# Optimization experiments

Hardware: AMD Instinct MI355X
Metric: run time of the kernel (lower is better)

The kernel has to match this reference:

```python
import jax, jax.numpy as jnp
import numpy as np

HEADS = 4
DIM_HEAD = 32
GROUPS = 32  # min(256//4, 32)
EPS = 1e-5


def setup_inputs() -> dict:
    key = jax.random.key(0)
    ks = jax.random.split(key, 6)
    B, C, H, W = 16, 256, 64, 64
    hidden = HEADS * DIM_HEAD  # 128
    return {
        "x": jax.random.normal(ks[0], (B, C, H, W), dtype=jnp.float32),
        "gn_w": jax.random.uniform(ks[1], (C,), dtype=jnp.float32),
        "gn_b": jax.random.normal(ks[2], (C,), dtype=jnp.float32) * 0.05,
        "qkv_w": jax.random.normal(ks[3], (3 * hidden, C), dtype=jnp.float32) * 0.05,
        "qkv_b": jax.random.normal(ks[4], (3 * hidden,), dtype=jnp.float32) * 0.05,
        "out_w": jax.random.normal(ks[5], (C, hidden), dtype=jnp.float32) * 0.05,
        "out_b": jnp.zeros((C,), dtype=jnp.float32),
    }


def _forward_single(x, gn_w, gn_b, qkv_w, qkv_b, out_w, out_b):
    # x: (c, h, w)
    c, h, w = x.shape
    # GroupNorm over (channels-in-group, h, w)
    xg = x.reshape(GROUPS, c // GROUPS, h, w)
    mean = xg.mean(axis=(1, 2, 3), keepdims=True)
    var = xg.var(axis=(1, 2, 3), keepdims=True)
    xn = ((xg - mean) * jax.lax.rsqrt(var + EPS)).reshape(c, h, w)
    xn = xn * gn_w[:, None, None] + gn_b[:, None, None]
    # 1x1 conv QKV projection
    qkv = jnp.einsum('oc,chw->ohw', qkv_w, xn) + qkv_b[:, None, None]
    qkv = qkv.reshape(3, HEADS, DIM_HEAD, h * w)
    q, k, v = qkv[0], qkv[1], qkv[2]
    k = jax.nn.softmax(k, axis=-1)  # softmax over spatial
    context = jnp.einsum('hdn,hen->hde', k, v)   # (heads, d, d)
    out = jnp.einsum('hde,hdn->hen', context, q)  # (heads, d, n)
    out = out.reshape(HEADS * DIM_HEAD, h, w)
    # 1x1 conv output projection
    return jnp.einsum('oc,chw->ohw', out_w, out) + out_b[:, None, None]


def reference(x, gn_w, gn_b, qkv_w, qkv_b, out_w, out_b):
    f = lambda xi: _forward_single(xi, gn_w, gn_b, qkv_w, qkv_b, out_w, out_b)
    return jax.vmap(f)(x)
```

## Files before the change

kernel.cpp:

```cpp
#include <hip/hip_runtime.h>
#include <stdint.h>

typedef unsigned short u16;
typedef __attribute__((ext_vector_type(8))) short bf16x8;
typedef __attribute__((ext_vector_type(4))) float f32x4;

#define B_   16
#define C_   256
#define HW_  4096
#define QR_  384
#define HID_ 128

__device__ __forceinline__ float b2f(u16 u) {
  union { uint32_t i; float f; } v; v.i = ((uint32_t)u) << 16; return v.f;
}
__device__ __forceinline__ u16 f2b(float f) {
  union { float f; uint32_t i; } v; v.f = f;
  uint32_t r = (v.i + 0x7FFFu + ((v.i >> 16) & 1u)) >> 16;
  return (u16)r;
}

__global__ __launch_bounds__(256) void gn_stats_conv_kernel(
    const float* __restrict__ x, const float* __restrict__ gnw,
    const float* __restrict__ gnb, float* __restrict__ scale,
    float* __restrict__ shiftv,
    const float* __restrict__ qkvw, u16* __restrict__ cqkvw)
{
  if (blockIdx.x >= 512) {
    int i = (blockIdx.x - 512) * 256 + threadIdx.x;
    float4 f = ((const float4*)qkvw)[i];
    ushort4 o;
    o.x = f2b(f.x); o.y = f2b(f.y); o.z = f2b(f.z); o.w = f2b(f.w);
    ((ushort4*)cqkvw)[i] = o;
    return;
  }
  int b = blockIdx.x >> 5, g = blockIdx.x & 31;
  const float* p = x + ((size_t)b * C_ + g * 8) * HW_;
  int t = threadIdx.x;
  float s = 0.f, sq = 0.f;
#pragma unroll
  for (int i = 0; i < 16; ++i) {
    float4 u0 = *(const float4*)(p + t * 8 + i * 2048);
    float4 u1 = *(const float4*)(p + t * 8 + i * 2048 + 4);
    s  += u0.x + u0.y + u0.z + u0.w + u1.x + u1.y + u1.z + u1.w;
    sq += u0.x*u0.x + u0.y*u0.y + u0.z*u0.z + u0.w*u0.w
        + u1.x*u1.x + u1.y*u1.y + u1.z*u1.z + u1.w*u1.w;
  }
#pragma unroll
  for (int off = 32; off > 0; off >>= 1) {
    s  += __shfl_down(s, off);
    sq += __shfl_down(sq, off);
  }
  __shared__ float ps[4], pq[4], mr[2];
  int lane = t & 63, w = t >> 6;
  if (lane == 0) { ps[w] = s; pq[w] = sq; }
  __syncthreads();
  if (t == 0) {
    float S = ps[0] + ps[1] + ps[2] + ps[3];
    float Q = pq[0] + pq[1] + pq[2] + pq[3];
    float mean = S * (1.f / 32768.f);
    float var  = Q * (1.f / 32768.f) - mean * mean;
    mr[0] = mean; mr[1] = rsqrtf(var + 1e-5f);
  }
  __syncthreads();
  if (t < 8) {
    int c = g * 8 + t;
    float sc = gnw[c] * mr[1];
    scale[b * C_ + c]  = sc;
    shiftv[b * C_ + c] = gnb[c] - mr[0] * sc;
  }
}

__global__ __launch_bounds__(256) void gn_transpose_kernel(
    const float* __restrict__ x, u16* __restrict__ dst,
    const float* __restrict__ scale, const float* __restrict__ shiftv)
{
  int nt = blockIdx.x, ct = blockIdx.y, b = blockIdx.z;
  const float* S = x + (size_t)b * C_ * HW_;
  u16* D = dst + (size_t)b * HW_ * C_;
  __shared__ __align__(16) u16 tile[64][136];
  int t = threadIdx.x;
  int n0 = nt * 128, c0 = ct * 64;
  int r = t >> 2, seg = (t & 3) * 32;
  float sc = scale[(size_t)b * C_ + c0 + r];
  float sh = shiftv[(size_t)b * C_ + c0 + r];
#pragma unroll
  for (int i = 0; i < 4; ++i) {
    const float* rp = S + (size_t)(c0 + r) * HW_ + n0 + seg + i * 8;
    float4 u0 = *(const float4*)(rp);
    float4 u1 = *(const float4*)(rp + 4);
    float f[8] = {u0.x, u0.y, u0.z, u0.w, u1.x, u1.y, u1.z, u1.w};
    uint4 o;
    uint32_t* op = (uint32_t*)&o;
#pragma unroll
    for (int j = 0; j < 4; ++j) {
      op[j] = (uint32_t)f2b(f[2 * j] * sc + sh)
            | ((uint32_t)f2b(f[2 * j + 1] * sc + sh) << 16);
    }
    *(uint4*)&tile[r][seg + i * 8] = o;
  }
  __syncthreads();
#pragma unroll
  for (int i = 0; i < 4; ++i) {
    int m = t * 4 + i;
    int n_l = m >> 3, cg = (m & 7) * 8;
    union { u16 v[8]; uint4 q; } pk;
#pragma unroll
    for (int e = 0; e < 8; ++e) pk.v[e] = tile[cg + e][n_l];
    *(uint4*)(D + (size_t)(n0 + n_l) * C_ + c0 + cg) = pk.q;
  }
}

__global__ __launch_bounds__(256) void qkv_gemm_kernel(
    const u16* __restrict__ A, const u16* __restrict__ Bt,
    const float* __restrict__ bias, u16* __restrict__ qkv,
    u16* __restrict__ q_t)
{
  const int K = C_;
  int nt = blockIdx.x, mt = blockIdx.y, b = blockIdx.z;
  const u16* Ab = A + (size_t)mt * 128 * K;
  const u16* Bb = Bt + (size_t)b * HW_ * C_ + (size_t)nt * 128 * K;
  __shared__ __align__(16) u16 smem[128 * 136];
  u16* lA = smem;
  u16* lB = smem + 8192;
  int t = threadIdx.x;
  int lane = t & 63, w = t >> 6;
  int quad = lane >> 4, l16 = lane & 15;
  int wm = (w >> 1) * 64, wn = (w & 1) * 64;
  f32x4 acc[4][4];
#pragma unroll
  for (int i = 0; i < 4; ++i)
#pragma unroll
    for (int j = 0; j < 4; ++j)
#pragma unroll
      for (int r = 0; r < 4; ++r) acc[i][j][r] = 0.f;

  for (int k0 = 0; k0 < K; k0 += 64) {
    __syncthreads();
#pragma unroll
    for (int q = 0; q < 4; ++q) {
      int ch = q * 256 + t;
      int row = ch >> 3, off = (ch & 7) * 8;
      __builtin_amdgcn_global_load_lds(
          (const __attribute__((address_space(1))) void*)(Ab + (size_t)row * K + k0 + off),
          (__attribute__((address_space(3))) void*)(lA + ch * 8), 16, 0, 0);
      __builtin_amdgcn_global_load_lds(
          (const __attribute__((address_space(1))) void*)(Bb + (size_t)row * K + k0 + off),
          (__attribute__((address_space(3))) void*)(lB + ch * 8), 16, 0, 0);
    }
    __syncthreads();
    const bf16x8* A8 = (const bf16x8*)lA;
    const bf16x8* B8 = (const bf16x8*)lB;
#pragma unroll
    for (int kk = 0; kk < 2; ++kk) {
      bf16x8 af[4], bfr[4];
#pragma unroll
      for (int i = 0; i < 4; ++i) af[i]  = A8[(wm + i * 16 + l16) * 8 + kk * 4 + quad];
#pragma unroll
      for (int j = 0; j < 4; ++j) bfr[j] = B8[(wn + j * 16 + l16) * 8 + kk * 4 + quad];
#pragma unroll
      for (int i = 0; i < 4; ++i)
#pragma unroll
        for (int j = 0; j < 4; ++j)
          acc[i][j] = __builtin_amdgcn_mfma_f32_16x16x32_bf16(af[i], bfr[j],
                                                              acc[i][j], 0, 0, 0);
    }
  }

  if (mt == 0) {
    __syncthreads();
#pragma unroll
    for (int i = 0; i < 4; ++i) {
      int o0 = wm + i * 16 + quad * 4;
      float b0 = bias[o0], b1 = bias[o0 + 1], b2 = bias[o0 + 2], b3 = bias[o0 + 3];
#pragma unroll
      for (int j = 0; j < 4; ++j) {
        int n_l = wn + j * 16 + l16;
        uint2 pk;
        pk.x = (uint32_t)f2b(acc[i][j][0] + b0) | ((uint32_t)f2b(acc[i][j][1] + b1) << 16);
        pk.y = (uint32_t)f2b(acc[i][j][2] + b2) | ((uint32_t)f2b(acc[i][j][3] + b3) << 16);
        *(uint2*)&smem[n_l * 136 + o0] = pk;
      }
    }
    __syncthreads();
    int n_l = t >> 1, half = t & 1;
    u16* dst = q_t + (size_t)b * HW_ * HID_ + (size_t)(nt * 128 + n_l) * HID_ + half * 64;
    const u16* srcp = smem + n_l * 136 + half * 64;
#pragma unroll
    for (int i = 0; i < 8; ++i)
      *(uint4*)(dst + i * 8) = *(const uint4*)(srcp + i * 8);
  } else {
#pragma unroll
    for (int i = 0; i < 4; ++i) {
#pragma unroll
      for (int rg = 0; rg < 4; ++rg) {
        int o = mt * 128 + wm + i * 16 + quad * 4 + rg;
        float bsv = bias[o];
        size_t rowbase = (size_t)b * QR_ * HW_ + (size_t)o * HW_;
#pragma unroll
        for (int j = 0; j < 4; ++j) {
          int n = nt * 128 + wn + j * 16 + l16;
          qkv[rowbase + n] = f2b(acc[i][j][rg] + bsv);
        }
      }
    }
  }
}

__global__ __launch_bounds__(1024) void ctxwf_kernel(
    const u16* __restrict__ qkv, const float* __restrict__ outw,
    u16* __restrict__ wf)
{
  int b = blockIdx.x >> 2, h = blockIdx.x & 3;
  const u16* kb = qkv + ((size_t)b * QR_ + 128 + h * 32) * HW_;
  const u16* vb = qkv + ((size_t)b * QR_ + 256 + h * 32) * HW_;
  int t = threadIdx.x;
  int w = t >> 6, lane = t & 63;
  int quad = lane >> 4, l16 = lane & 15;
  __shared__ float part[16][1024];
  __shared__ float cs[1024];
  __shared__ float2 sred[1024];
  __shared__ float sinv[32];
  f32x4 acc[2][2];
#pragma unroll
  for (int i = 0; i < 2; ++i)
#pragma unroll
    for (int j = 0; j < 2; ++j)
#pragma unroll
      for (int r = 0; r < 4; ++r) acc[i][j][r] = 0.f;
  float s0 = 0.f, s1 = 0.f;
  int kbase = w * 256;
  for (int it = 0; it < 8; ++it) {
    int n0 = kbase + it * 32 + quad * 8;
    bf16x8 k0 = *(const bf16x8*)(kb + (size_t)l16 * HW_ + n0);
    bf16x8 k1 = *(const bf16x8*)(kb + (size_t)(16 + l16) * HW_ + n0);
    bf16x8 v0 = *(const bf16x8*)(vb + (size_t)l16 * HW_ + n0);
    bf16x8 v1 = *(const bf16x8*)(vb + (size_t)(16 + l16) * HW_ + n0);
    bf16x8 a0, a1;
    const u16* k0p = (const u16*)&k0; u16* a0p = (u16*)&a0;
    const u16* k1p = (const u16*)&k1; u16* a1p = (u16*)&a1;
#pragma unroll
    for (int e = 0; e < 8; ++e) {
      float e0 = __expf(b2f(k0p[e]));
      float e1 = __expf(b2f(k1p[e]));
      s0 += e0; s1 += e1;
      a0p[e] = f2b(e0);
      a1p[e] = f2b(e1);
    }
    acc[0][0] = __builtin_amdgcn_mfma_f32_16x16x32_bf16(a0, v0, acc[0][0], 0, 0, 0);
    acc[0][1] = __builtin_amdgcn_mfma_f32_16x16x32_bf16(a0, v1, acc[0][1], 0, 0, 0);
    acc[1][0] = __builtin_amdgcn_mfma_f32_16x16x32_bf16(a1, v0, acc[1][0], 0, 0, 0);
    acc[1][1] = __builtin_amdgcn_mfma_f32_16x16x32_bf16(a1, v1, acc[1][1], 0, 0, 0);
  }
#pragma unroll
  for (int i = 0; i < 2; ++i)
#pragma unroll
    for (int j = 0; j < 2; ++j)
#pragma unroll
      for (int r = 0; r < 4; ++r) {
        int d = i * 16 + quad * 4 + r;
        int e = j * 16 + l16;
        part[w][d * 32 + e] = acc[i][j][r];
      }
  sred[t] = make_float2(s0, s1);
  __syncthreads();
  {
    float a = 0.f;
#pragma unroll
    for (int ww = 0; ww < 16; ++ww) a += part[ww][t];
    cs[t] = a;
  }
  if (t < 32) {
    int d = t, lsel = d & 15;
    float ssum = 0.f;
#pragma unroll
    for (int ww = 0; ww < 16; ++ww)
#pragma unroll
      for (int q = 0; q < 4; ++q) {
        float2 v2 = sred[ww * 64 + q * 16 + lsel];
        ssum += (d < 16) ? v2.x : v2.y;
      }
    sinv[d] = 1.f / ssum;
  }
  __syncthreads();

  int o = t & 255, dg = t >> 8;
  const float* wr = outw + (size_t)o * HID_ + h * 32;
  float wv[32];
#pragma unroll
  for (int e = 0; e < 32; ++e) wv[e] = wr[e];
  union { u16 v[8]; uint4 q; } pk;
#pragma unroll
  for (int dd = 0; dd < 8; ++dd) {
    int d = dg * 8 + dd;
    float a = 0.f;
#pragma unroll
    for (int e = 0; e < 32; ++e) a += wv[e] * cs[d * 32 + e];
    pk.v[dd] = f2b(a * sinv[d]);
  }
  *(uint4*)(wf + ((size_t)b * C_ + o) * HID_ + h * 32 + dg * 8) = pk.q;
}

__global__ __launch_bounds__(256) void out_gemm_kernel(
    const u16* __restrict__ A, const u16* __restrict__ Bt,
    const float* __restrict__ bias, float* __restrict__ Cout)
{
  const int K = HID_;
  int nt = blockIdx.x, mt = blockIdx.y, b = blockIdx.z;
  const u16* Ab = A + (size_t)b * C_ * HID_ + (size_t)mt * 128 * K;
  const u16* Bb = Bt + (size_t)b * HW_ * HID_ + (size_t)nt * 128 * K;
  __shared__ __align__(16) u16 lA[128 * 64];
  __shared__ __align__(16) u16 lB[128 * 64];
  int t = threadIdx.x;
  int lane = t & 63, w = t >> 6;
  int quad = lane >> 4, l16 = lane & 15;
  int wm = (w >> 1) * 64, wn = (w & 1) * 64;
  f32x4 acc[4][4];
#pragma unroll
  for (int i = 0; i < 4; ++i)
#pragma unroll
    for (int j = 0; j < 4; ++j)
#pragma unroll
      for (int r = 0; r < 4; ++r) acc[i][j][r] = 0.f;

  for (int k0 = 0; k0 < K; k0 += 64) {
    __syncthreads();
#pragma unroll
    for (int q = 0; q < 4; ++q) {
      int ch = q * 256 + t;
      int row = ch >> 3, off = (ch & 7) * 8;
      __builtin_amdgcn_global_load_lds(
          (const __attribute__((address_space(1))) void*)(Ab + (size_t)row * K + k0 + off),
          (__attribute__((address_space(3))) void*)(lA + ch * 8), 16, 0, 0);
      __builtin_amdgcn_global_load_lds(
          (const __attribute__((address_space(1))) void*)(Bb + (size_t)row * K + k0 + off),
          (__attribute__((address_space(3))) void*)(lB + ch * 8), 16, 0, 0);
    }
    __syncthreads();
    const bf16x8* A8 = (const bf16x8*)lA;
    const bf16x8* B8 = (const bf16x8*)lB;
#pragma unroll
    for (int kk = 0; kk < 2; ++kk) {
      bf16x8 af[4], bfr[4];
#pragma unroll
      for (int i = 0; i < 4; ++i) af[i]  = A8[(wm + i * 16 + l16) * 8 + kk * 4 + quad];
#pragma unroll
      for (int j = 0; j < 4; ++j) bfr[j] = B8[(wn + j * 16 + l16) * 8 + kk * 4 + quad];
#pragma unroll
      for (int i = 0; i < 4; ++i)
#pragma unroll
        for (int j = 0; j < 4; ++j)
          acc[i][j] = __builtin_amdgcn_mfma_f32_16x16x32_bf16(af[i], bfr[j],
                                                              acc[i][j], 0, 0, 0);
    }
  }
#pragma unroll
  for (int i = 0; i < 4; ++i) {
#pragma unroll
    for (int rg = 0; rg < 4; ++rg) {
      int o = mt * 128 + wm + i * 16 + quad * 4 + rg;
      float bsv = bias[o];
      size_t rowbase = (size_t)b * C_ * HW_ + (size_t)o * HW_;
#pragma unroll
      for (int j = 0; j < 4; ++j) {
        int n = nt * 128 + wn + j * 16 + l16;
        Cout[rowbase + n] = acc[i][j][rg] + bsv;
      }
    }
  }
}

extern "C" void kernel_launch(void* const* d_in, const int* in_sizes, int n_in,
                              void* d_out, int out_size, void* d_ws, size_t ws_size,
                              hipStream_t stream)
{
  const float* x    = (const float*)d_in[0];
  const float* gnw  = (const float*)d_in[1];
  const float* gnb  = (const float*)d_in[2];
  const float* qkvw = (const float*)d_in[3];
  const float* qkvb = (const float*)d_in[4];
  const float* outw = (const float*)d_in[5];
  const float* outb = (const float*)d_in[6];

  char* p = (char*)d_ws;
  float* scale  = (float*)p;            p += (size_t)B_ * C_ * 4;
  float* shiftv = (float*)p;            p += (size_t)B_ * C_ * 4;
  u16* cqkvw = (u16*)p;                 p += (size_t)QR_ * C_ * 2;
  u16* xn_t  = (u16*)p;                 p += (size_t)B_ * HW_ * C_ * 2;
  u16* qkv   = (u16*)p;                 p += (size_t)B_ * QR_ * HW_ * 2;
  u16* q_t   = (u16*)p;                 p += (size_t)B_ * HW_ * HID_ * 2;
  u16* wf    = (u16*)p;

  gn_stats_conv_kernel<<<608, 256, 0, stream>>>(x, gnw, gnb, scale, shiftv,
                                                qkvw, cqkvw);
  gn_transpose_kernel<<<dim3(32, 4, 16), 256, 0, stream>>>(x, xn_t, scale, shiftv);
  qkv_gemm_kernel<<<dim3(32, 3, 16), 256, 0, stream>>>(cqkvw, xn_t, qkvb, qkv, q_t);
  ctxwf_kernel<<<64, 1024, 0, stream>>>(qkv, outw, wf);
  out_gemm_kernel<<<dim3(32, 2, 16), 256, 0, stream>>>(wf, q_t, outb, (float*)d_out);
}
```

Measured before the change: 206.9 us.

## Fuse K/V projection with softmax-exp and context accumulation, avoiding K/V materialisation

Splits the QKV GEMM into a Q-only GEMM and a new K/V kernel that computes K and V tiles, applies exp to K, and multiplies the tiles in shared memory to produce per-tile partial contexts and softmax sums. This removes the bf16 write and re-read of the full K/V tensors and spreads the context reduction over 512 blocks instead of 64. A small fold kernel then sums the partials, folds the V bias into the output-weight product and builds the fused weight. The cost is extra partial-buffer traffic and a third launch. K is computed without its bias, which is safe because softmax over spatial positions is unchanged by a per-row constant shift, so no max-subtraction is done.

```diff
diff --git a/kernel.cpp b/kernel.cpp
--- a/kernel.cpp
+++ b/kernel.cpp
@@ -111,14 +111,13 @@
   }
 }
 
-__global__ __launch_bounds__(256) void qkv_gemm_kernel(
+__global__ __launch_bounds__(256) void q_gemm_kernel(
     const u16* __restrict__ A, const u16* __restrict__ Bt,
-    const float* __restrict__ bias, u16* __restrict__ qkv,
-    u16* __restrict__ q_t)
+    const float* __restrict__ bias, u16* __restrict__ q_t)
 {
   const int K = C_;
-  int nt = blockIdx.x, mt = blockIdx.y, b = blockIdx.z;
-  const u16* Ab = A + (size_t)mt * 128 * K;
+  int nt = blockIdx.x, b = blockIdx.y;
+  const u16* Ab = A;
   const u16* Bb = Bt + (size_t)b * HW_ * C_ + (size_t)nt * 128 * K;
   __shared__ __align__(16) u16 smem[128 * 136];
   u16* lA = smem;
@@ -167,138 +166,228 @@
     }
   }
 
-  if (mt == 0) {
-    __syncthreads();
-#pragma unroll
-    for (int i = 0; i < 4; ++i) {
-      int o0 = wm + i * 16 + quad * 4;
-      float b0 = bias[o0], b1 = bias[o0 + 1], b2 = bias[o0 + 2], b3 = bias[o0 + 3];
-#pragma unroll
-      for (int j = 0; j < 4; ++j) {
-        int n_l = wn + j * 16 + l16;
-        uint2 pk;
-        pk.x = (uint32_t)f2b(acc[i][j][0] + b0) | ((uint32_t)f2b(acc[i][j][1] + b1) << 16);
-        pk.y = (uint32_t)f2b(acc[i][j][2] + b2) | ((uint32_t)f2b(acc[i][j][3] + b3) << 16);
-        *(uint2*)&smem[n_l * 136 + o0] = pk;
+  __syncthreads();
+#pragma unroll
+  for (int i = 0; i < 4; ++i) {
+    int o0 = wm + i * 16 + quad * 4;
+    float b0 = bias[o0], b1 = bias[o0 + 1], b2 = bias[o0 + 2], b3 = bias[o0 + 3];
+#pragma unroll
+    for (int j = 0; j < 4; ++j) {
+      int n_l = wn + j * 16 + l16;
+      uint2 pk;
+      pk.x = (uint32_t)f2b(acc[i][j][0] + b0) | ((uint32_t)f2b(acc[i][j][1] + b1) << 16);
+      pk.y = (uint32_t)f2b(acc[i][j][2] + b2) | ((uint32_t)f2b(acc[i][j][3] + b3) << 16);
+      *(uint2*)&smem[n_l * 136 + o0] = pk;
+    }
+  }
+  __syncthreads();
+  int n_l = t >> 1, half = t & 1;
+  u16* dst = q_t + (size_t)b * HW_ * HID_ + (size_t)(nt * 128 + n_l) * HID_ + half * 64;
+  const u16* srcp = smem + n_l * 136 + half * 64;
+#pragma unroll
+  for (int i = 0; i < 8; ++i)
+    *(uint4*)(dst + i * 8) = *(const uint4*)(srcp + i * 8);
+}
+
+__global__ __launch_bounds__(512) void kv_ctx_kernel(
+    const u16* __restrict__ A,
+    const u16* __restrict__ Bt,
+    float* __restrict__ ctx_part,
+    float* __restrict__ s_part)
+{
+  const int K = C_;
+  int nt = blockIdx.x, b = blockIdx.y;
+  const u16* Ab = A;
+  const u16* Bb = Bt + (size_t)b * HW_ * C_ + (size_t)nt * 128 * K;
+  __shared__ __align__(16) union {
+    struct { u16 lA[256 * 64]; u16 lB[128 * 64]; } st;
+    struct { u16 ek[128][136]; u16 vv[128][136]; float sred[2][128]; } ep;
+    float cred[4096];
+  } sm;
+  int t = threadIdx.x;
+  int lane = t & 63, w = t >> 6;
+  int quad = lane >> 4, l16 = lane & 15;
+  int wm = (w >> 1) * 64, wn = (w & 1) * 64;
+  f32x4 acc[4][4];
+#pragma unroll
+  for (int i = 0; i < 4; ++i)
+#pragma unroll
+    for (int j = 0; j < 4; ++j)
+#pragma unroll
+      for (int r = 0; r < 4; ++r) acc[i][j][r] = 0.f;
+
+  for (int k0 = 0; k0 < K; k0 += 64) {
+    __syncthreads();
+#pragma unroll
+    for (int q = 0; q < 4; ++q) {
+      int ch = q * 512 + t;
+      int row = ch >> 3, off = (ch & 7) * 8;
+      __builtin_amdgcn_global_load_lds(
+          (const __attribute__((address_space(1))) void*)(Ab + (size_t)row * K + k0 + off),
+          (__attribute__((address_space(3))) void*)(sm.st.lA + ch * 8), 16, 0, 0);
+    }
+#pragma unroll
+    for (int q = 0; q < 2; ++q) {
+      int ch = q * 512 + t;
+      int row = ch >> 3, off = (ch & 7) * 8;
+      __builtin_amdgcn_global_load_lds(
+          (const __attribute__((address_space(1))) void*)(Bb + (size_t)row * K + k0 + off),
+          (__attribute__((address_space(3))) void*)(sm.st.lB + ch * 8), 16, 0, 0);
+    }
+    __syncthreads();
+    const bf16x8* A8 = (const bf16x8*)sm.st.lA;
+    const bf16x8* B8 = (const bf16x8*)sm.st.lB;
+#pragma unroll
+    for (int kk = 0; kk < 2; ++kk) {
+      bf16x8 af[4], bfr[4];
+#pragma unroll
+      for (int i = 0; i < 4; ++i) af[i]  = A8[(wm + i * 16 + l16) * 8 + kk * 4 + quad];
+#pragma unroll
+      for (int j = 0; j < 4; ++j) bfr[j] = B8[(wn + j * 16 + l16) * 8 + kk * 4 + quad];
+#pragma unroll
+      for (int i = 0; i < 4; ++i)
+#pragma unroll
+        for (int j = 0; j < 4; ++j)
+          acc[i][j] = __builtin_amdgcn_mfma_f32_16x16x32_bf16(af[i], bfr[j],
+                                                              acc[i][j], 0, 0, 0);
+    }
+  }
+
+  __syncthreads();
+  int h = w >> 1, nh = w & 1;
+  if (w < 4) {
+    float sl[4][4];
+#pragma unroll
+    for (int i = 0; i < 4; ++i)
+#pragma unroll
+      for (int r = 0; r < 4; ++r) sl[i][r] = 0.f;
+#pragma unroll
+    for (int i = 0; i < 4; ++i)
+#pragma unroll
+      for (int j = 0; j < 4; ++j)
+#pragma unroll
+        for (int r = 0; r < 4; ++r) {
+          float e = __expf(acc[i][j][r]);
+          sl[i][r] += e;
+          sm.ep.ek[wm + i * 16 + quad * 4 + r][wn + j * 16 + l16] = f2b(e);
+        }
+#pragma unroll
+    for (int i = 0; i < 4; ++i)
+#pragma unroll
+      for (int r = 0; r < 4; ++r) {
+        float v = sl[i][r];
+        v += __shfl_xor(v, 1);
+        v += __shfl_xor(v, 2);
+        v += __shfl_xor(v, 4);
+        v += __shfl_xor(v, 8);
+        if (l16 == 0) sm.ep.sred[nh][wm + i * 16 + quad * 4 + r] = v;
       }
-    }
-    __syncthreads();
-    int n_l = t >> 1, half = t & 1;
-    u16* dst = q_t + (size_t)b * HW_ * HID_ + (size_t)(nt * 128 + n_l) * HID_ + half * 64;
-    const u16* srcp = smem + n_l * 136 + half * 64;
-#pragma unroll
-    for (int i = 0; i < 8; ++i)
-      *(uint4*)(dst + i * 8) = *(const uint4*)(srcp + i * 8);
   } else {
 #pragma unroll
-    for (int i = 0; i < 4; ++i) {
-#pragma unroll
-      for (int rg = 0; rg < 4; ++rg) {
-        int o = mt * 128 + wm + i * 16 + quad * 4 + rg;
-        float bsv = bias[o];
-        size_t rowbase = (size_t)b * QR_ * HW_ + (size_t)o * HW_;
-#pragma unroll
-        for (int j = 0; j < 4; ++j) {
-          int n = nt * 128 + wn + j * 16 + l16;
-          qkv[rowbase + n] = f2b(acc[i][j][rg] + bsv);
-        }
-      }
-    }
-  }
-}
-
-__global__ __launch_bounds__(1024) void ctxwf_kernel(
-    const u16* __restrict__ qkv, const float* __restrict__ outw,
+    for (int i = 0; i < 4; ++i)
+#pragma unroll
+      for (int j = 0; j < 4; ++j)
+#pragma unroll
+        for (int r = 0; r < 4; ++r)
+          sm.ep.vv[wm - 128 + i * 16 + quad * 4 + r][wn + j * 16 + l16] =
+              f2b(acc[i][j][r]);
+  }
+  __syncthreads();
+  if (t < 128)
+    s_part[((size_t)b * 32 + nt) * 128 + t] = sm.ep.sred[0][t] + sm.ep.sred[1][t];
+
+  f32x4 c2[2][2];
+#pragma unroll
+  for (int i = 0; i < 2; ++i)
+#pragma unroll
+    for (int j = 0; j < 2; ++j)
+#pragma unroll
+      for (int r = 0; r < 4; ++r) c2[i][j][r] = 0.f;
+#pragma unroll
+  for (int kk = 0; kk < 2; ++kk) {
+    bf16x8 ae[2], be[2];
+#pragma unroll
+    for (int i = 0; i < 2; ++i)
+      ae[i] = *(const bf16x8*)&sm.ep.ek[h * 32 + i * 16 + l16][nh * 64 + kk * 32 + quad * 8];
+#pragma unroll
+    for (int j = 0; j < 2; ++j)
+      be[j] = *(const bf16x8*)&sm.ep.vv[h * 32 + j * 16 + l16][nh * 64 + kk * 32 + quad * 8];
+#pragma unroll
+    for (int i = 0; i < 2; ++i)
+#pragma unroll
+      for (int j = 0; j < 2; ++j)
+        c2[i][j] = __builtin_amdgcn_mfma_f32_16x16x32_bf16(ae[i], be[j], c2[i][j], 0, 0, 0);
+  }
+  __syncthreads();
+  if (nh == 0) {
+#pragma unroll
+    for (int i = 0; i < 2; ++i)
+#pragma unroll
+      for (int j = 0; j < 2; ++j)
+#pragma unroll
+        for (int r = 0; r < 4; ++r)
+          sm.cred[h * 1024 + (i * 16 + quad * 4 + r) * 32 + j * 16 + l16] = c2[i][j][r];
+  }
+  __syncthreads();
+  if (nh == 1) {
+#pragma unroll
+    for (int i = 0; i < 2; ++i)
+#pragma unroll
+      for (int j = 0; j < 2; ++j)
+#pragma unroll
+        for (int r = 0; r < 4; ++r)
+          sm.cred[h * 1024 + (i * 16 + quad * 4 + r) * 32 + j * 16 + l16] += c2[i][j][r];
+  }
+  __syncthreads();
+  float4* dst = (float4*)(ctx_part + ((size_t)b * 32 + nt) * 4096);
+  const float4* src4 = (const float4*)sm.cred;
+  dst[t] = src4[t];
+  dst[t + 512] = src4[t + 512];
+}
+
+__global__ __launch_bounds__(256) void fold_kernel(
+    const float* __restrict__ ctx_part, const float* __restrict__ s_part,
+    const float* __restrict__ outw, const float* __restrict__ qkvb,
     u16* __restrict__ wf)
 {
   int b = blockIdx.x >> 2, h = blockIdx.x & 3;
-  const u16* kb = qkv + ((size_t)b * QR_ + 128 + h * 32) * HW_;
-  const u16* vb = qkv + ((size_t)b * QR_ + 256 + h * 32) * HW_;
-  int t = threadIdx.x;
-  int w = t >> 6, lane = t & 63;
-  int quad = lane >> 4, l16 = lane & 15;
-  __shared__ float part[16][1024];
+  int t = threadIdx.x;
   __shared__ float cs[1024];
-  __shared__ float2 sred[1024];
   __shared__ float sinv[32];
-  f32x4 acc[2][2];
-#pragma unroll
-  for (int i = 0; i < 2; ++i)
-#pragma unroll
-    for (int j = 0; j < 2; ++j)
-#pragma unroll
-      for (int r = 0; r < 4; ++r) acc[i][j][r] = 0.f;
-  float s0 = 0.f, s1 = 0.f;
-  int kbase = w * 256;
-  for (int it = 0; it < 8; ++it) {
-    int n0 = kbase + it * 32 + quad * 8;
-    bf16x8 k0 = *(const bf16x8*)(kb + (size_t)l16 * HW_ + n0);
-    bf16x8 k1 = *(const bf16x8*)(kb + (size_t)(16 + l16) * HW_ + n0);
-    bf16x8 v0 = *(const bf16x8*)(vb + (size_t)l16 * HW_ + n0);
-    bf16x8 v1 = *(const bf16x8*)(vb + (size_t)(16 + l16) * HW_ + n0);
-    bf16x8 a0, a1;
-    const u16* k0p = (const u16*)&k0; u16* a0p = (u16*)&a0;
-    const u16* k1p = (const u16*)&k1; u16* a1p = (u16*)&a1;
-#pragma unroll
-    for (int e = 0; e < 8; ++e) {
-      float e0 = __expf(b2f(k0p[e]));
-      float e1 = __expf(b2f(k1p[e]));
-      s0 += e0; s1 += e1;
-      a0p[e] = f2b(e0);
-      a1p[e] = f2b(e1);
-    }
-    acc[0][0] = __builtin_amdgcn_mfma_f32_16x16x32_bf16(a0, v0, acc[0][0], 0, 0, 0);
-    acc[0][1] = __builtin_amdgcn_mfma_f32_16x16x32_bf16(a0, v1, acc[0][1], 0, 0, 0);
-    acc[1][0] = __builtin_amdgcn_mfma_f32_16x16x32_bf16(a1, v0, acc[1][0], 0, 0, 0);
-    acc[1][1] = __builtin_amdgcn_mfma_f32_16x16x32_bf16(a1, v1, acc[1][1], 0, 0, 0);
-  }
-#pragma unroll
-  for (int i = 0; i < 2; ++i)
-#pragma unroll
-    for (int j = 0; j < 2; ++j)
-#pragma unroll
-      for (int r = 0; r < 4; ++r) {
-        int d = i * 16 + quad * 4 + r;
-        int e = j * 16 + l16;
-        part[w][d * 32 + e] = acc[i][j][r];
-      }
-  sred[t] = make_float2(s0, s1);
-  __syncthreads();
-  {
-    float a = 0.f;
-#pragma unroll
-    for (int ww = 0; ww < 16; ++ww) a += part[ww][t];
-    cs[t] = a;
-  }
+  const float* cp = ctx_part + ((size_t)b * 32) * 4096 + h * 1024;
+  float4 aa = make_float4(0.f, 0.f, 0.f, 0.f);
+  for (int ntb = 0; ntb < 32; ++ntb) {
+    float4 v = *(const float4*)(cp + (size_t)ntb * 4096 + t * 4);
+    aa.x += v.x; aa.y += v.y; aa.z += v.z; aa.w += v.w;
+  }
+  *(float4*)&cs[t * 4] = aa;
   if (t < 32) {
-    int d = t, lsel = d & 15;
     float ssum = 0.f;
-#pragma unroll
-    for (int ww = 0; ww < 16; ++ww)
-#pragma unroll
-      for (int q = 0; q < 4; ++q) {
-        float2 v2 = sred[ww * 64 + q * 16 + lsel];
-        ssum += (d < 16) ? v2.x : v2.y;
-      }
-    sinv[d] = 1.f / ssum;
-  }
-  __syncthreads();
-
-  int o = t & 255, dg = t >> 8;
+    for (int ntb = 0; ntb < 32; ++ntb)
+      ssum += s_part[((size_t)b * 32 + ntb) * 128 + h * 32 + t];
+    sinv[t] = 1.f / ssum;
+  }
+  __syncthreads();
+  int o = t;
   const float* wr = outw + (size_t)o * HID_ + h * 32;
   float wv[32];
-#pragma unroll
-  for (int e = 0; e < 32; ++e) wv[e] = wr[e];
-  union { u16 v[8]; uint4 q; } pk;
-#pragma unroll
-  for (int dd = 0; dd < 8; ++dd) {
-    int d = dg * 8 + dd;
+  float cb = 0.f;
+#pragma unroll
+  for (int e = 0; e < 32; ++e) {
+    wv[e] = wr[e];
+    cb += wv[e] * qkvb[256 + h * 32 + e];
+  }
+  union { u16 v[32]; uint4 q[4]; } pk;
+#pragma unroll
+  for (int d = 0; d < 32; ++d) {
     float a = 0.f;
 #pragma unroll
     for (int e = 0; e < 32; ++e) a += wv[e] * cs[d * 32 + e];
-    pk.v[dd] = f2b(a * sinv[d]);
-  }
-  *(uint4*)(wf + ((size_t)b * C_ + o) * HID_ + h * 32 + dg * 8) = pk.q;
+    pk.v[d] = f2b(a * sinv[d] + cb);
+  }
+  uint4* dp = (uint4*)(wf + ((size_t)b * C_ + o) * HID_ + h * 32);
+#pragma unroll
+  for (int i = 0; i < 4; ++i) dp[i] = pk.q[i];
 }
 
 __global__ __launch_bounds__(256) void out_gemm_kernel(
@@ -387,14 +476,16 @@
   float* shiftv = (float*)p;            p += (size_t)B_ * C_ * 4;
   u16* cqkvw = (u16*)p;                 p += (size_t)QR_ * C_ * 2;
   u16* xn_t  = (u16*)p;                 p += (size_t)B_ * HW_ * C_ * 2;
-  u16* qkv   = (u16*)p;                 p += (size_t)B_ * QR_ * HW_ * 2;
   u16* q_t   = (u16*)p;                 p += (size_t)B_ * HW_ * HID_ * 2;
-  u16* wf    = (u16*)p;
+  u16* wf    = (u16*)p;                 p += (size_t)B_ * C_ * HID_ * 2;
+  float* ctxp = (float*)p;              p += (size_t)B_ * 32 * 4 * 1024 * 4;
+  float* sp   = (float*)p;
 
   gn_stats_conv_kernel<<<608, 256, 0, stream>>>(x, gnw, gnb, scale, shiftv,
                                                 qkvw, cqkvw);
   gn_transpose_kernel<<<dim3(32, 4, 16), 256, 0, stream>>>(x, xn_t, scale, shiftv);
-  qkv_gemm_kernel<<<dim3(32, 3, 16), 256, 0, stream>>>(cqkvw, xn_t, qkvb, qkv, q_t);
-  ctxwf_kernel<<<64, 1024, 0, stream>>>(qkv, outw, wf);
+  q_gemm_kernel<<<dim3(32, 16), 256, 0, stream>>>(cqkvw, xn_t, qkvb, q_t);
+  kv_ctx_kernel<<<dim3(32, 16), 512, 0, stream>>>(cqkvw + 128 * C_, xn_t, ctxp, sp);
+  fold_kernel<<<64, 256, 0, stream>>>(ctxp, sp, outw, qkvb, wf);
   out_gemm_kernel<<<dim3(32, 2, 16), 256, 0, stream>>>(wf, q_t, outb, (float*)d_out);
 }
```

Measured after the change: 195.9 us. 1.06x faster.
